# Kernel tuning notes

Hardware: AMD Instinct MI355X
Metric: run time of the kernel (lower is better)

Reference implementation:

```python
import jax, jax.numpy as jnp
import numpy as np

E, T, D_H, D_I, R = 8, 4096, 2048, 5632, 128


def setup_inputs() -> dict:
    key = jax.random.key(0)
    ks = jax.random.split(key, 12)
    s = 0.02
    return {
        "x": jax.random.normal(ks[0], (T, D_H), dtype=jnp.float32),
        "expert_idx": jax.random.randint(ks[1], (T,), 0, E),
        # gate: hidden -> intermediate
        "gate_A": jax.random.normal(ks[2], (E, R, D_H), dtype=jnp.float32) * s,
        "gate_C": jax.random.normal(ks[3], (R, R), dtype=jnp.float32) * s,
        "gate_B": jax.random.normal(ks[4], (E, D_I, R), dtype=jnp.float32) * s,
        # up: hidden -> intermediate
        "up_A": jax.random.normal(ks[5], (E, R, D_H), dtype=jnp.float32) * s,
        "up_C": jax.random.normal(ks[6], (R, R), dtype=jnp.float32) * s,
        "up_B": jax.random.normal(ks[7], (E, D_I, R), dtype=jnp.float32) * s,
        # down: intermediate -> hidden, with per-expert bias
        "down_A": jax.random.normal(ks[8], (E, R, D_I), dtype=jnp.float32) * s,
        "down_C": jax.random.normal(ks[9], (R, R), dtype=jnp.float32) * s,
        "down_B": jax.random.normal(ks[10], (E, D_H, R), dtype=jnp.float32) * s,
        "down_bias": jax.random.normal(ks[11], (E, D_H), dtype=jnp.float32) * s,
    }


def _shared_core(x, A, C, B, onehot_et):
    # x: [t, d_in]; A: [e, r, d_in]; C: [r, r]; B: [e, d_out, r]; onehot_et: [e, t]
    # per-token expert weight W_e = B_e @ C @ A_e; mask early so zeros propagate
    h = jnp.einsum('td,erd->etr', x, A) * onehot_et[:, :, None]  # [e, t, r]
    h = jnp.einsum('etr,sr->ets', h, C)                           # [e, t, r]
    return jnp.einsum('ets,eds->td', h, B)                        # [t, d_out]


def reference(x, expert_idx, gate_A, gate_C, gate_B, up_A, up_C, up_B,
              down_A, down_C, down_B, down_bias):
    onehot = jax.nn.one_hot(expert_idx, E, dtype=x.dtype).T  # [E, T]
    g = jax.nn.silu(_shared_core(x, gate_A, gate_C, gate_B, onehot))  # [T, D_I]
    u = _shared_core(x, up_A, up_C, up_B, onehot)                     # [T, D_I]
    down = _shared_core(g * u, down_A, down_C, down_B, onehot)        # [T, D_H]
    return down + down_bias[expert_idx]
```

## Files before the change

kernel.cpp:

```cpp
#include <hip/hip_runtime.h>
#include <hip/hip_bf16.h>

#define E_  8
#define T_  4096
#define DH_ 2048
#define DI_ 5632
#define R_  128
#define TILE_ 64
#define NT_ 72
#define TPMAX_ (NT_*TILE_)

typedef short bf16x8 __attribute__((ext_vector_type(8)));
typedef short bf16x4 __attribute__((ext_vector_type(4)));
typedef float f32x4 __attribute__((ext_vector_type(4)));

#define MFMA(a, b, c) __builtin_amdgcn_mfma_f32_16x16x32_bf16((a), (b), (c), 0, 0, 0)

__device__ __forceinline__ unsigned short f2bf(float f) {
  union { float f; unsigned u; } v; v.f = f;
  return (unsigned short)((v.u + 0x7fffu + ((v.u >> 16) & 1u)) >> 16);
}

__device__ __forceinline__ bf16x8 cvt8(float4 a, float4 b) {
  bf16x8 o;
  o[0] = (short)f2bf(a.x); o[1] = (short)f2bf(a.y);
  o[2] = (short)f2bf(a.z); o[3] = (short)f2bf(a.w);
  o[4] = (short)f2bf(b.x); o[5] = (short)f2bf(b.y);
  o[6] = (short)f2bf(b.z); o[7] = (short)f2bf(b.w);
  return o;
}

__device__ __forceinline__ int tile_expert(int s0, const int* off) {
  int e = 0;
#pragma unroll
  for (int q = 1; q < E_; q++) if (s0 >= off[q]) e = q;
  return e;
}

__global__ __launch_bounds__(1024) void k_route(
    const int* __restrict__ idx, int* __restrict__ off, int* __restrict__ tok)
{
  __shared__ int cnt[E_], cur[E_], offs[E_ + 1];
  const int tid = threadIdx.x;
  if (tid < E_) cnt[tid] = 0;
  __syncthreads();
  for (int t = tid; t < T_; t += 1024) atomicAdd(&cnt[idx[t]], 1);
  __syncthreads();
  if (tid == 0) {
    int a = 0;
    for (int e = 0; e < E_; e++) {
      offs[e] = a; cur[e] = a;
      a += ((cnt[e] + TILE_ - 1) / TILE_) * TILE_;
    }
    offs[E_] = a;
  }
  __syncthreads();
  if (tid <= E_) off[tid] = offs[tid];
  for (int t = tid; t < T_; t += 1024) {
    int p = atomicAdd(&cur[idx[t]], 1);
    tok[p] = t;
  }
}

__global__ __launch_bounds__(256) void k_cvt(
    const float* __restrict__ gA, const float* __restrict__ uA,
    const float* __restrict__ gB, const float* __restrict__ uB,
    const float* __restrict__ dA, const float* __restrict__ dB,
    const float* __restrict__ gC, const float* __restrict__ uC,
    const float* __restrict__ dC,
    short* __restrict__ gAb, short* __restrict__ uAb,
    short* __restrict__ gBb, short* __restrict__ uBb,
    short* __restrict__ dAb, short* __restrict__ dBb,
    short* __restrict__ gCb, short* __restrict__ uCb,
    short* __restrict__ dCb)
{
  long i = (long)(blockIdx.x * 256 + threadIdx.x) * 4;
  const float* s; short* d;
  if      (i <  4194304) { if (i < 2097152) { s = gA; d = gAb; } else { s = uA; d = uAb; i -= 2097152; } }
  else if (i <  9961472) { s = gB; d = gBb; i -= 4194304; }
  else if (i < 15728640) { s = uB; d = uBb; i -= 9961472; }
  else if (i < 21495808) { s = dA; d = dAb; i -= 15728640; }
  else if (i < 23592960) { s = dB; d = dBb; i -= 21495808; }
  else if (i < 23609344) { s = gC; d = gCb; i -= 23592960; }
  else if (i < 23625728) { s = uC; d = uCb; i -= 23609344; }
  else if (i < 23642112) { s = dC; d = dCb; i -= 23625728; }
  else return;
  float4 v = *(const float4*)(s + i);
  bf16x4 o;
  o[0] = (short)f2bf(v.x); o[1] = (short)f2bf(v.y);
  o[2] = (short)f2bf(v.z); o[3] = (short)f2bf(v.w);
  *(bf16x4*)(d + i) = o;
}

__global__ __launch_bounds__(256) void k_gather(
    const float* __restrict__ x, const int* __restrict__ tok,
    short* __restrict__ Xb)
{
  const int p = blockIdx.x;
  const int t = tok[p];
  const int c = threadIdx.x * 8;
  bf16x8 o;
  if (t >= 0) {
    float4 v0 = *(const float4*)(x + (size_t)t * DH_ + c);
    float4 v1 = *(const float4*)(x + (size_t)t * DH_ + c + 4);
    o = cvt8(v0, v1);
  } else {
    o = (bf16x8){0, 0, 0, 0, 0, 0, 0, 0};
  }
  *(bf16x8*)(Xb + (size_t)p * DH_ + c) = o;
}

__global__ __launch_bounds__(256) void k_stage1(
    const short* __restrict__ Xb,
    const short* __restrict__ gAb, const short* __restrict__ uAb,
    const int* __restrict__ off, float* __restrict__ Hp)
{
  const int s0 = blockIdx.x * TILE_;
  if (s0 >= off[E_]) return;
  const int e = tile_expert(s0, off);
  const int y = blockIdx.y, kc = blockIdx.z;
  const short* A = (y ? uAb : gAb) + (size_t)e * R_ * DH_ + kc * 512;

  const int tid = threadIdx.x;
  const int lane = tid & 63, wv = tid >> 6;
  const int col = lane & 15, quad = lane >> 4;

  const short* xb = Xb + (size_t)(s0 + col) * DH_ + kc * 512 + quad * 8;
  const short* ab = A + (size_t)(wv * 32 + col) * DH_ + quad * 8;

  f32x4 acc[4][2] = {};
#pragma unroll 4
  for (int k0 = 0; k0 < 512; k0 += 32) {
    bf16x8 b0 = *(const bf16x8*)(ab + k0);
    bf16x8 b1 = *(const bf16x8*)(ab + (size_t)16 * DH_ + k0);
#pragma unroll
    for (int m = 0; m < 4; m++) {
      bf16x8 a = *(const bf16x8*)(xb + (size_t)m * 16 * DH_ + k0);
      acc[m][0] = MFMA(a, b0, acc[m][0]);
      acc[m][1] = MFMA(a, b1, acc[m][1]);
    }
  }
  float* O = Hp + (size_t)(y * 4 + kc) * TPMAX_ * R_;
#pragma unroll
  for (int m = 0; m < 4; m++)
#pragma unroll
    for (int nl = 0; nl < 2; nl++)
#pragma unroll
      for (int r = 0; r < 4; r++)
        O[(size_t)(s0 + m * 16 + quad * 4 + r) * R_ + (wv * 2 + nl) * 16 + col] =
            acc[m][nl][r];
}

__global__ __launch_bounds__(256) void k_stage1b(
    const float* __restrict__ Hp,
    const short* __restrict__ gCb, const short* __restrict__ uCb,
    const int* __restrict__ off,
    short* __restrict__ Hgb, short* __restrict__ Hub)
{
  const int s0 = blockIdx.x * TILE_;
  if (s0 >= off[E_]) return;
  const int y = blockIdx.y;
  const short* C = y ? uCb : gCb;
  short* H = y ? Hub : Hgb;

  __shared__ short h1s[64][136];
  const int tid = threadIdx.x;
  {
    const int lg = tid >> 2, lq = (tid & 3) * 32;
    const float* base = Hp + ((size_t)y * 4 * TPMAX_ + s0 + lg) * R_ + lq;
    float s[32] = {};
#pragma unroll
    for (int kc = 0; kc < 4; kc++) {
      const float* p = base + (size_t)kc * TPMAX_ * R_;
#pragma unroll
      for (int q = 0; q < 8; q++) {
        float4 v = *(const float4*)(p + q * 4);
        s[q * 4 + 0] += v.x; s[q * 4 + 1] += v.y;
        s[q * 4 + 2] += v.z; s[q * 4 + 3] += v.w;
      }
    }
#pragma unroll
    for (int j = 0; j < 32; j++) h1s[lg][lq + j] = (short)f2bf(s[j]);
  }
  __syncthreads();

  const int lane = tid & 63, wv = tid >> 6;
  const int col = lane & 15, quad = lane >> 4;
  f32x4 acc2[4][2] = {};
#pragma unroll
  for (int kk = 0; kk < 4; kk++) {
    bf16x8 b[2];
#pragma unroll
    for (int nl = 0; nl < 2; nl++)
      b[nl] = *(const bf16x8*)(C + (size_t)((wv * 2 + nl) * 16 + col) * R_ +
                               kk * 32 + quad * 8);
#pragma unroll
    for (int m = 0; m < 4; m++) {
      bf16x8 a = *(const bf16x8*)&h1s[m * 16 + col][kk * 32 + quad * 8];
      acc2[m][0] = MFMA(a, b[0], acc2[m][0]);
      acc2[m][1] = MFMA(a, b[1], acc2[m][1]);
    }
  }
#pragma unroll
  for (int m = 0; m < 4; m++)
#pragma unroll
    for (int nl = 0; nl < 2; nl++)
#pragma unroll
      for (int r = 0; r < 4; r++)
        H[(size_t)(s0 + m * 16 + quad * 4 + r) * R_ + (wv * 2 + nl) * 16 + col] =
            (short)f2bf(acc2[m][nl][r]);
}

__global__ __launch_bounds__(256) void k_stage2(
    const short* __restrict__ Hgb, const short* __restrict__ Hub,
    const short* __restrict__ gBb, const short* __restrict__ uBb,
    const short* __restrict__ dAb,
    const int* __restrict__ off, float* __restrict__ Hd1)
{
  const int s0 = blockIdx.x * TILE_;
  if (s0 >= off[E_]) return;
  const int e = tile_expert(s0, off);
  const int i0 = blockIdx.y * 512;
  const short* Bg = gBb + (size_t)e * DI_ * R_;
  const short* Bu = uBb + (size_t)e * DI_ * R_;
  const short* Ad = dAb + (size_t)e * R_ * DI_;

  __shared__ short hgs[64][136];
  __shared__ short hus[64][136];
  __shared__ short ZT[64][136];

  const int tid = threadIdx.x;
  const int lane = tid & 63, wv = tid >> 6;
  const int col = lane & 15, quad = lane >> 4;

  {
    const int row = tid >> 2, seg = (tid & 3) * 32;
    const short* pg = Hgb + (size_t)(s0 + row) * R_ + seg;
    const short* pu = Hub + (size_t)(s0 + row) * R_ + seg;
#pragma unroll
    for (int q = 0; q < 4; q++) {
      *(bf16x8*)&hgs[row][seg + q * 8] = *(const bf16x8*)(pg + q * 8);
      *(bf16x8*)&hus[row][seg + q * 8] = *(const bf16x8*)(pu + q * 8);
    }
  }
  __syncthreads();

  f32x4 dacc[4][2] = {};

  for (int sc = 0; sc < 4; sc++) {
    const int ib = i0 + sc * 128;
    f32x4 gacc[4][2] = {}, uacc[4][2] = {};
#pragma unroll
    for (int kk = 0; kk < 4; kk++) {
      bf16x8 bg[2], bu[2];
#pragma unroll
      for (int nl = 0; nl < 2; nl++) {
        size_t bo = (size_t)(ib + (wv * 2 + nl) * 16 + col) * R_ + kk * 32 + quad * 8;
        bg[nl] = *(const bf16x8*)(Bg + bo);
        bu[nl] = *(const bf16x8*)(Bu + bo);
      }
#pragma unroll
      for (int m = 0; m < 4; m++) {
        bf16x8 ag = *(const bf16x8*)&hgs[m * 16 + col][kk * 32 + quad * 8];
        bf16x8 au = *(const bf16x8*)&hus[m * 16 + col][kk * 32 + quad * 8];
#pragma unroll
        for (int nl = 0; nl < 2; nl++) {
          gacc[m][nl] = MFMA(ag, bg[nl], gacc[m][nl]);
          uacc[m][nl] = MFMA(au, bu[nl], uacc[m][nl]);
        }
      }
    }
    __syncthreads();
#pragma unroll
    for (int m = 0; m < 4; m++)
#pragma unroll
      for (int nl = 0; nl < 2; nl++)
#pragma unroll
        for (int r = 0; r < 4; r++) {
          float g = gacc[m][nl][r];
          float z = (g / (1.0f + __expf(-g))) * uacc[m][nl][r];
          ZT[m * 16 + quad * 4 + r][(wv * 2 + nl) * 16 + col] = (short)f2bf(z);
        }
    __syncthreads();
#pragma unroll
    for (int kk2 = 0; kk2 < 4; kk2++) {
      bf16x8 ba[2];
#pragma unroll
      for (int nl = 0; nl < 2; nl++)
        ba[nl] = *(const bf16x8*)(Ad + (size_t)((wv * 2 + nl) * 16 + col) * DI_ +
                                  ib + kk2 * 32 + quad * 8);
#pragma unroll
      for (int m = 0; m < 4; m++) {
        bf16x8 za = *(const bf16x8*)&ZT[m * 16 + col][kk2 * 32 + quad * 8];
        dacc[m][0] = MFMA(za, ba[0], dacc[m][0]);
        dacc[m][1] = MFMA(za, ba[1], dacc[m][1]);
      }
    }
  }
#pragma unroll
  for (int m = 0; m < 4; m++)
#pragma unroll
    for (int nl = 0; nl < 2; nl++)
#pragma unroll
      for (int r = 0; r < 4; r++)
        atomicAdd(&Hd1[(size_t)(s0 + m * 16 + quad * 4 + r) * R_ + (wv * 2 + nl) * 16 + col],
                  dacc[m][nl][r]);
}

__global__ __launch_bounds__(256) void k_stage3(
    const float* __restrict__ Hd1, const short* __restrict__ dCb,
    const short* __restrict__ dBb, const float* __restrict__ dbias,
    const int* __restrict__ off, const int* __restrict__ tok,
    float* __restrict__ out)
{
  const int s0 = blockIdx.x * TILE_;
  if (s0 >= off[E_]) return;
  const int e = tile_expert(s0, off);
  const int d0 = blockIdx.y * 128;

  __shared__ short h2s[64][136];
  const int tid = threadIdx.x;
  const int lane = tid & 63, wv = tid >> 6;
  const int col = lane & 15, quad = lane >> 4;

  f32x4 acc2[4][2] = {};
#pragma unroll
  for (int kk = 0; kk < 4; kk++) {
    bf16x8 b[2];
#pragma unroll
    for (int nl = 0; nl < 2; nl++)
      b[nl] = *(const bf16x8*)(dCb + (size_t)((wv * 2 + nl) * 16 + col) * R_ +
                               kk * 32 + quad * 8);
#pragma unroll
    for (int m = 0; m < 4; m++) {
      const float* hp = Hd1 + (size_t)(s0 + m * 16 + col) * R_ + kk * 32 + quad * 8;
      float4 v0 = *(const float4*)hp;
      float4 v1 = *(const float4*)(hp + 4);
      bf16x8 a = cvt8(v0, v1);
      acc2[m][0] = MFMA(a, b[0], acc2[m][0]);
      acc2[m][1] = MFMA(a, b[1], acc2[m][1]);
    }
  }
#pragma unroll
  for (int m = 0; m < 4; m++)
#pragma unroll
    for (int nl = 0; nl < 2; nl++)
#pragma unroll
      for (int r = 0; r < 4; r++)
        h2s[m * 16 + quad * 4 + r][(wv * 2 + nl) * 16 + col] = (short)f2bf(acc2[m][nl][r]);
  __syncthreads();

  f32x4 acc3[4][2] = {};
#pragma unroll
  for (int kk = 0; kk < 4; kk++) {
    bf16x8 b[2];
#pragma unroll
    for (int nl = 0; nl < 2; nl++)
      b[nl] = *(const bf16x8*)(dBb + (size_t)e * DH_ * R_ +
                               (size_t)(d0 + (wv * 2 + nl) * 16 + col) * R_ +
                               kk * 32 + quad * 8);
#pragma unroll
    for (int m = 0; m < 4; m++) {
      bf16x8 a = *(const bf16x8*)&h2s[m * 16 + col][kk * 32 + quad * 8];
      acc3[m][0] = MFMA(a, b[0], acc3[m][0]);
      acc3[m][1] = MFMA(a, b[1], acc3[m][1]);
    }
  }
  float bias[2];
#pragma unroll
  for (int nl = 0; nl < 2; nl++)
    bias[nl] = dbias[(size_t)e * DH_ + d0 + (wv * 2 + nl) * 16 + col];
#pragma unroll
  for (int m = 0; m < 4; m++)
#pragma unroll
    for (int r = 0; r < 4; r++) {
      int t = tok[s0 + m * 16 + quad * 4 + r];
      if (t < 0) continue;
#pragma unroll
      for (int nl = 0; nl < 2; nl++) {
        int d = d0 + (wv * 2 + nl) * 16 + col;
        out[(size_t)t * DH_ + d] = acc3[m][nl][r] + bias[nl];
      }
    }
}

extern "C" void kernel_launch(void* const* d_in, const int* in_sizes, int n_in,
                              void* d_out, int out_size, void* d_ws, size_t ws_size,
                              hipStream_t stream)
{
  (void)in_sizes; (void)n_in; (void)out_size; (void)ws_size;
  const float* x     = (const float*)d_in[0];
  const int*   idx   = (const int*)d_in[1];
  const float* gA    = (const float*)d_in[2];
  const float* gC    = (const float*)d_in[3];
  const float* gBw   = (const float*)d_in[4];
  const float* uA    = (const float*)d_in[5];
  const float* uC    = (const float*)d_in[6];
  const float* uBw   = (const float*)d_in[7];
  const float* dA    = (const float*)d_in[8];
  const float* dC    = (const float*)d_in[9];
  const float* dBw   = (const float*)d_in[10];
  const float* dbias = (const float*)d_in[11];
  float* out = (float*)d_out;

  char* ws = (char*)d_ws;
  int* off = (int*)ws;
  int* tok = (int*)(ws + 512);
  float* Hd1 = (float*)(ws + 32768);
  float* Hp  = (float*)(ws + 2392064);
  short* Xb  = (short*)(ws + 21266432);
  short* Hgb = (short*)(ws + 40140800);
  short* Hub = (short*)(ws + 41320448);
  short* gAb = (short*)(ws + 42500096);
  short* uAb = (short*)(ws + 46694400);
  short* gBb = (short*)(ws + 50888704);
  short* uBb = (short*)(ws + 62423040);
  short* dAb = (short*)(ws + 73957376);
  short* dBb = (short*)(ws + 85491712);
  short* gCb = (short*)(ws + 89686016);
  short* uCb = (short*)(ws + 89718784);
  short* dCb = (short*)(ws + 89751552);

  hipMemsetAsync(tok, 0xFF, TPMAX_ * sizeof(int), stream);
  hipMemsetAsync(Hd1, 0, (size_t)TPMAX_ * R_ * sizeof(float), stream);

  k_cvt    <<<dim3(23088), 256, 0, stream>>>(gA, uA, gBw, uBw, dA, dBw, gC, uC, dC,
                                             gAb, uAb, gBb, uBb, dAb, dBb, gCb, uCb, dCb);
  k_route  <<<1, 1024, 0, stream>>>(idx, off, tok);
  k_gather <<<dim3(TPMAX_), 256, 0, stream>>>(x, tok, Xb);
  k_stage1 <<<dim3(NT_, 2, 4), 256, 0, stream>>>(Xb, gAb, uAb, off, Hp);
  k_stage1b<<<dim3(NT_, 2), 256, 0, stream>>>(Hp, gCb, uCb, off, Hgb, Hub);
  k_stage2 <<<dim3(NT_, 11), 256, 0, stream>>>(Hgb, Hub, gBb, uBb, dAb, off, Hd1);
  k_stage3 <<<dim3(NT_, 16), 256, 0, stream>>>(Hd1, dCb, dBb, dbias, off, tok, out);
}
```

Baseline: 334.7 us.

## Make stage2/stage3 weight-stationary per expert, split C-apply into own kernel

```diff
diff --git a/kernel.cpp b/kernel.cpp
--- a/kernel.cpp
+++ b/kernel.cpp
@@ -211,66 +211,68 @@
             (short)f2bf(acc2[m][nl][r]);
 }
 
-__global__ __launch_bounds__(256) void k_stage2(
+__global__ __launch_bounds__(256, 2) void k_stage2(
     const short* __restrict__ Hgb, const short* __restrict__ Hub,
     const short* __restrict__ gBb, const short* __restrict__ uBb,
     const short* __restrict__ dAb,
     const int* __restrict__ off, float* __restrict__ Hd1)
 {
-  const int s0 = blockIdx.x * TILE_;
-  if (s0 >= off[E_]) return;
-  const int e = tile_expert(s0, off);
-  const int i0 = blockIdx.y * 512;
+  const int e = blockIdx.x;
+  const int i0 = blockIdx.y * 128;
+  const int lo = off[e], hi = off[e + 1];
+  if (lo >= hi) return;
   const short* Bg = gBb + (size_t)e * DI_ * R_;
   const short* Bu = uBb + (size_t)e * DI_ * R_;
   const short* Ad = dAb + (size_t)e * R_ * DI_;
 
+  const int tid = threadIdx.x;
+  const int lane = tid & 63, wv = tid >> 6;
+  const int col = lane & 15, quad = lane >> 4;
+
+  bf16x8 wg[4][2], wu[4][2], wa[4][2];
+#pragma unroll
+  for (int kk = 0; kk < 4; kk++)
+#pragma unroll
+    for (int nl = 0; nl < 2; nl++) {
+      size_t bo = (size_t)(i0 + (wv * 2 + nl) * 16 + col) * R_ + kk * 32 + quad * 8;
+      wg[kk][nl] = *(const bf16x8*)(Bg + bo);
+      wu[kk][nl] = *(const bf16x8*)(Bu + bo);
+      wa[kk][nl] = *(const bf16x8*)(Ad + (size_t)((wv * 2 + nl) * 16 + col) * DI_ +
+                                    i0 + kk * 32 + quad * 8);
+    }
+
   __shared__ short hgs[64][136];
   __shared__ short hus[64][136];
   __shared__ short ZT[64][136];
 
-  const int tid = threadIdx.x;
-  const int lane = tid & 63, wv = tid >> 6;
-  const int col = lane & 15, quad = lane >> 4;
-
-  {
-    const int row = tid >> 2, seg = (tid & 3) * 32;
-    const short* pg = Hgb + (size_t)(s0 + row) * R_ + seg;
-    const short* pu = Hub + (size_t)(s0 + row) * R_ + seg;
-#pragma unroll
-    for (int q = 0; q < 4; q++) {
-      *(bf16x8*)&hgs[row][seg + q * 8] = *(const bf16x8*)(pg + q * 8);
-      *(bf16x8*)&hus[row][seg + q * 8] = *(const bf16x8*)(pu + q * 8);
-    }
-  }
-  __syncthreads();
-
-  f32x4 dacc[4][2] = {};
-
-  for (int sc = 0; sc < 4; sc++) {
-    const int ib = i0 + sc * 128;
+  for (int s0 = lo; s0 < hi; s0 += TILE_) {
+    {
+      const int row = tid >> 2, seg = (tid & 3) * 32;
+      const short* pg = Hgb + (size_t)(s0 + row) * R_ + seg;
+      const short* pu = Hub + (size_t)(s0 + row) * R_ + seg;
+#pragma unroll
+      for (int q = 0; q < 4; q++) {
+        *(bf16x8*)&hgs[row][seg + q * 8] = *(const bf16x8*)(pg + q * 8);
+        *(bf16x8*)&hus[row][seg + q * 8] = *(const bf16x8*)(pu + q * 8);
+      }
+    }
+    __syncthreads();
+
     f32x4 gacc[4][2] = {}, uacc[4][2] = {};
 #pragma unroll
-    for (int kk = 0; kk < 4; kk++) {
-      bf16x8 bg[2], bu[2];
-#pragma unroll
-      for (int nl = 0; nl < 2; nl++) {
-        size_t bo = (size_t)(ib + (wv * 2 + nl) * 16 + col) * R_ + kk * 32 + quad * 8;
-        bg[nl] = *(const bf16x8*)(Bg + bo);
-        bu[nl] = *(const bf16x8*)(Bu + bo);
-      }
+    for (int kk = 0; kk < 4; kk++)
 #pragma unroll
       for (int m = 0; m < 4; m++) {
         bf16x8 ag = *(const bf16x8*)&hgs[m * 16 + col][kk * 32 + quad * 8];
         bf16x8 au = *(const bf16x8*)&hus[m * 16 + col][kk * 32 + quad * 8];
 #pragma unroll
         for (int nl = 0; nl < 2; nl++) {
-          gacc[m][nl] = MFMA(ag, bg[nl], gacc[m][nl]);
-          uacc[m][nl] = MFMA(au, bu[nl], uacc[m][nl]);
+          gacc[m][nl] = MFMA(ag, wg[kk][nl], gacc[m][nl]);
+          uacc[m][nl] = MFMA(au, wu[kk][nl], uacc[m][nl]);
         }
       }
-    }
     __syncthreads();
+
 #pragma unroll
     for (int m = 0; m < 4; m++)
 #pragma unroll
@@ -282,106 +284,118 @@
           ZT[m * 16 + quad * 4 + r][(wv * 2 + nl) * 16 + col] = (short)f2bf(z);
         }
     __syncthreads();
-#pragma unroll
-    for (int kk2 = 0; kk2 < 4; kk2++) {
-      bf16x8 ba[2];
-#pragma unroll
-      for (int nl = 0; nl < 2; nl++)
-        ba[nl] = *(const bf16x8*)(Ad + (size_t)((wv * 2 + nl) * 16 + col) * DI_ +
-                                  ib + kk2 * 32 + quad * 8);
+
+    f32x4 dacc[4][2] = {};
+#pragma unroll
+    for (int kk2 = 0; kk2 < 4; kk2++)
 #pragma unroll
       for (int m = 0; m < 4; m++) {
         bf16x8 za = *(const bf16x8*)&ZT[m * 16 + col][kk2 * 32 + quad * 8];
-        dacc[m][0] = MFMA(za, ba[0], dacc[m][0]);
-        dacc[m][1] = MFMA(za, ba[1], dacc[m][1]);
-      }
-    }
-  }
-#pragma unroll
-  for (int m = 0; m < 4; m++)
-#pragma unroll
-    for (int nl = 0; nl < 2; nl++)
-#pragma unroll
-      for (int r = 0; r < 4; r++)
-        atomicAdd(&Hd1[(size_t)(s0 + m * 16 + quad * 4 + r) * R_ + (wv * 2 + nl) * 16 + col],
-                  dacc[m][nl][r]);
-}
-
-__global__ __launch_bounds__(256) void k_stage3(
+        dacc[m][0] = MFMA(za, wa[kk2][0], dacc[m][0]);
+        dacc[m][1] = MFMA(za, wa[kk2][1], dacc[m][1]);
+      }
+#pragma unroll
+    for (int m = 0; m < 4; m++)
+#pragma unroll
+      for (int nl = 0; nl < 2; nl++)
+#pragma unroll
+        for (int r = 0; r < 4; r++)
+          atomicAdd(&Hd1[(size_t)(s0 + m * 16 + quad * 4 + r) * R_ +
+                         (wv * 2 + nl) * 16 + col],
+                    dacc[m][nl][r]);
+  }
+}
+
+__global__ __launch_bounds__(256) void k_applyCd(
     const float* __restrict__ Hd1, const short* __restrict__ dCb,
-    const short* __restrict__ dBb, const float* __restrict__ dbias,
-    const int* __restrict__ off, const int* __restrict__ tok,
-    float* __restrict__ out)
+    const int* __restrict__ off, short* __restrict__ Hd2b)
 {
   const int s0 = blockIdx.x * TILE_;
   if (s0 >= off[E_]) return;
-  const int e = tile_expert(s0, off);
-  const int d0 = blockIdx.y * 128;
-
-  __shared__ short h2s[64][136];
   const int tid = threadIdx.x;
   const int lane = tid & 63, wv = tid >> 6;
   const int col = lane & 15, quad = lane >> 4;
 
-  f32x4 acc2[4][2] = {};
-#pragma unroll
-  for (int kk = 0; kk < 4; kk++) {
-    bf16x8 b[2];
-#pragma unroll
-    for (int nl = 0; nl < 2; nl++)
-      b[nl] = *(const bf16x8*)(dCb + (size_t)((wv * 2 + nl) * 16 + col) * R_ +
-                               kk * 32 + quad * 8);
+  bf16x8 wc[4][2];
+#pragma unroll
+  for (int kk = 0; kk < 4; kk++)
+#pragma unroll
+    for (int nl = 0; nl < 2; nl++)
+      wc[kk][nl] = *(const bf16x8*)(dCb + (size_t)((wv * 2 + nl) * 16 + col) * R_ +
+                                    kk * 32 + quad * 8);
+
+  f32x4 acc[4][2] = {};
+#pragma unroll
+  for (int kk = 0; kk < 4; kk++)
 #pragma unroll
     for (int m = 0; m < 4; m++) {
       const float* hp = Hd1 + (size_t)(s0 + m * 16 + col) * R_ + kk * 32 + quad * 8;
       float4 v0 = *(const float4*)hp;
       float4 v1 = *(const float4*)(hp + 4);
       bf16x8 a = cvt8(v0, v1);
-      acc2[m][0] = MFMA(a, b[0], acc2[m][0]);
-      acc2[m][1] = MFMA(a, b[1], acc2[m][1]);
-    }
-  }
+      acc[m][0] = MFMA(a, wc[kk][0], acc[m][0]);
+      acc[m][1] = MFMA(a, wc[kk][1], acc[m][1]);
+    }
 #pragma unroll
   for (int m = 0; m < 4; m++)
 #pragma unroll
     for (int nl = 0; nl < 2; nl++)
 #pragma unroll
       for (int r = 0; r < 4; r++)
-        h2s[m * 16 + quad * 4 + r][(wv * 2 + nl) * 16 + col] = (short)f2bf(acc2[m][nl][r]);
-  __syncthreads();
-
-  f32x4 acc3[4][2] = {};
-#pragma unroll
-  for (int kk = 0; kk < 4; kk++) {
-    bf16x8 b[2];
-#pragma unroll
-    for (int nl = 0; nl < 2; nl++)
-      b[nl] = *(const bf16x8*)(dBb + (size_t)e * DH_ * R_ +
-                               (size_t)(d0 + (wv * 2 + nl) * 16 + col) * R_ +
-                               kk * 32 + quad * 8);
-#pragma unroll
-    for (int m = 0; m < 4; m++) {
-      bf16x8 a = *(const bf16x8*)&h2s[m * 16 + col][kk * 32 + quad * 8];
-      acc3[m][0] = MFMA(a, b[0], acc3[m][0]);
-      acc3[m][1] = MFMA(a, b[1], acc3[m][1]);
-    }
-  }
+        Hd2b[(size_t)(s0 + m * 16 + quad * 4 + r) * R_ + (wv * 2 + nl) * 16 + col] =
+            (short)f2bf(acc[m][nl][r]);
+}
+
+__global__ __launch_bounds__(256, 2) void k_stage3(
+    const short* __restrict__ Hd2b, const short* __restrict__ dBb,
+    const float* __restrict__ dbias,
+    const int* __restrict__ off, const int* __restrict__ tok,
+    float* __restrict__ out)
+{
+  const int e = blockIdx.x;
+  const int d0 = blockIdx.y * 128;
+  const int lo = off[e], hi = off[e + 1];
+  const int tid = threadIdx.x;
+  const int lane = tid & 63, wv = tid >> 6;
+  const int col = lane & 15, quad = lane >> 4;
+
+  bf16x8 wb[4][2];
+#pragma unroll
+  for (int kk = 0; kk < 4; kk++)
+#pragma unroll
+    for (int nl = 0; nl < 2; nl++)
+      wb[kk][nl] = *(const bf16x8*)(dBb + (size_t)e * DH_ * R_ +
+                                    (size_t)(d0 + (wv * 2 + nl) * 16 + col) * R_ +
+                                    kk * 32 + quad * 8);
   float bias[2];
 #pragma unroll
   for (int nl = 0; nl < 2; nl++)
     bias[nl] = dbias[(size_t)e * DH_ + d0 + (wv * 2 + nl) * 16 + col];
-#pragma unroll
-  for (int m = 0; m < 4; m++)
-#pragma unroll
-    for (int r = 0; r < 4; r++) {
-      int t = tok[s0 + m * 16 + quad * 4 + r];
-      if (t < 0) continue;
-#pragma unroll
-      for (int nl = 0; nl < 2; nl++) {
-        int d = d0 + (wv * 2 + nl) * 16 + col;
-        out[(size_t)t * DH_ + d] = acc3[m][nl][r] + bias[nl];
-      }
-    }
+
+  for (int s0 = lo + (int)blockIdx.z * TILE_; s0 < hi; s0 += 4 * TILE_) {
+    f32x4 acc[4][2] = {};
+#pragma unroll
+    for (int kk = 0; kk < 4; kk++)
+#pragma unroll
+      for (int m = 0; m < 4; m++) {
+        bf16x8 a = *(const bf16x8*)(Hd2b + (size_t)(s0 + m * 16 + col) * R_ +
+                                    kk * 32 + quad * 8);
+        acc[m][0] = MFMA(a, wb[kk][0], acc[m][0]);
+        acc[m][1] = MFMA(a, wb[kk][1], acc[m][1]);
+      }
+#pragma unroll
+    for (int m = 0; m < 4; m++)
+#pragma unroll
+      for (int r = 0; r < 4; r++) {
+        int t = tok[s0 + m * 16 + quad * 4 + r];
+        if (t < 0) continue;
+#pragma unroll
+        for (int nl = 0; nl < 2; nl++) {
+          int d = d0 + (wv * 2 + nl) * 16 + col;
+          out[(size_t)t * DH_ + d] = acc[m][nl][r] + bias[nl];
+        }
+      }
+  }
 }
 
 extern "C" void kernel_launch(void* const* d_in, const int* in_sizes, int n_in,
@@ -411,15 +425,16 @@
   short* Xb  = (short*)(ws + 21266432);
   short* Hgb = (short*)(ws + 40140800);
   short* Hub = (short*)(ws + 41320448);
-  short* gAb = (short*)(ws + 42500096);
-  short* uAb = (short*)(ws + 46694400);
-  short* gBb = (short*)(ws + 50888704);
-  short* uBb = (short*)(ws + 62423040);
-  short* dAb = (short*)(ws + 73957376);
-  short* dBb = (short*)(ws + 85491712);
-  short* gCb = (short*)(ws + 89686016);
-  short* uCb = (short*)(ws + 89718784);
-  short* dCb = (short*)(ws + 89751552);
+  short* Hd2b= (short*)(ws + 42500096);
+  short* gAb = (short*)(ws + 43679744);
+  short* uAb = (short*)(ws + 47874048);
+  short* gBb = (short*)(ws + 52068352);
+  short* uBb = (short*)(ws + 63602688);
+  short* dAb = (short*)(ws + 75137024);
+  short* dBb = (short*)(ws + 86671360);
+  short* gCb = (short*)(ws + 90865664);
+  short* uCb = (short*)(ws + 90898432);
+  short* dCb = (short*)(ws + 90931200);
 
   hipMemsetAsync(tok, 0xFF, TPMAX_ * sizeof(int), stream);
   hipMemsetAsync(Hd1, 0, (size_t)TPMAX_ * R_ * sizeof(float), stream);
@@ -430,6 +445,7 @@
   k_gather <<<dim3(TPMAX_), 256, 0, stream>>>(x, tok, Xb);
   k_stage1 <<<dim3(NT_, 2, 4), 256, 0, stream>>>(Xb, gAb, uAb, off, Hp);
   k_stage1b<<<dim3(NT_, 2), 256, 0, stream>>>(Hp, gCb, uCb, off, Hgb, Hub);
-  k_stage2 <<<dim3(NT_, 11), 256, 0, stream>>>(Hgb, Hub, gBb, uBb, dAb, off, Hd1);
-  k_stage3 <<<dim3(NT_, 16), 256, 0, stream>>>(Hd1, dCb, dBb, dbias, off, tok, out);
-}
+  k_stage2 <<<dim3(E_, 44), 256, 0, stream>>>(Hgb, Hub, gBb, uBb, dAb, off, Hd1);
+  k_applyCd<<<dim3(NT_), 256, 0, stream>>>(Hd1, dCb, off, Hd2b);
+  k_stage3 <<<dim3(E_, 16, 4), 256, 0, stream>>>(Hd2b, dBb, dbias, off, tok, out);
+}
```

New measurement: 349.7 us. +4.5%, slower.
